# Performance work log

Measured on AMD Instinct MI355X. Metric: run time of the kernel, lower is better.

Reference implementation:

```python
import jax, jax.numpy as jnp
import numpy as np

NUM_CLASSES = 64
FEAT_DIM = 128
LAMBDA_INTER = 1.0
LAMBDA_INTRA = 1.0
MARGIN = 2.0
BATCH = 1_000_000


def setup_inputs() -> dict:
    key = jax.random.key(0)
    k1, k2 = jax.random.split(key)
    features = jax.random.normal(k1, (BATCH, FEAT_DIM), dtype=jnp.float32)
    targets = jax.random.randint(k2, (BATCH,), 0, NUM_CLASSES, dtype=jnp.int32)
    return {"features": features, "targets": targets}


def reference(features, targets):
    C, D = NUM_CLASSES, FEAT_DIM
    B = features.shape[0]
    # per-class scatter-mean centroids
    sums = jax.ops.segment_sum(features, targets, num_segments=C)      # [C, D]
    counts = jax.ops.segment_sum(jnp.ones((B,), features.dtype), targets,
                                 num_segments=C)                        # [C]
    counts = jnp.clip(counts, 1.0)
    centers = sums / counts[:, None]                                    # [C, D]
    # intra-class variance: mean over batch of ||f_i - center_{t_i}||^2
    diff = features - centers[targets]                                   # [B, D]
    intra_loss = jnp.sum(diff * diff) / B
    # inter-class hinge on pairwise squared centroid distances (i < j)
    cd = centers[:, None, :] - centers[None, :, :]                       # [C, C, D]
    d2 = jnp.sum(cd * cd, axis=-1)                                       # [C, C]
    weights = jnp.ones((C, C), features.dtype).at[1, 2].set(2.0)
    upper = jnp.triu(jnp.ones((C, C), features.dtype), k=1)
    hinge = jnp.maximum(MARGIN - d2, 0.0)
    n_pairs = C * (C - 1) // 2
    inter_loss = jnp.sum(weights * hinge * upper) / n_pairs
    return LAMBDA_INTRA * intra_loss + LAMBDA_INTER * inter_loss
```

## Files before the change

kernel.cpp:

```cpp
#include <hip/hip_runtime.h>

#define BATCH 1000000
#define C 64
#define D 128
#define NPAIRS 2016
#define CHUNK 16

__global__ __launch_bounds__(128) void stage1_kernel(
        const float* __restrict__ feat, const int* __restrict__ targets,
        float* __restrict__ pSums, float* __restrict__ pCnt,
        double* __restrict__ pSq, int nB) {
    __shared__ float sAcc[C * D];
    __shared__ double sRed[128];

    const int tid = threadIdx.x;
    for (int i = tid; i < C * D; i += 128) sAcc[i] = 0.0f;
    __syncthreads();

    const int nchunks = BATCH / CHUNK;

    float lsq  = 0.0f;
    float lcnt = 0.0f;

    float fA[CHUNK], fB[CHUNK];
    int   tA[CHUNK], tB[CHUNK];

    int ch = blockIdx.x;
    {
        const int r0 = ch * CHUNK;
#pragma unroll
        for (int u = 0; u < CHUNK; u++) tA[u] = targets[r0 + u];
#pragma unroll
        for (int u = 0; u < CHUNK; u++) fA[u] = feat[(size_t)(r0 + u) * D + tid];
    }

    for (;;) {
        const int chN = ch + nB;
        const bool more = chN < nchunks;
        if (more) {
            const int r0 = chN * CHUNK;
#pragma unroll
            for (int u = 0; u < CHUNK; u++) tB[u] = targets[r0 + u];
#pragma unroll
            for (int u = 0; u < CHUNK; u++) fB[u] = feat[(size_t)(r0 + u) * D + tid];
        }
        __builtin_amdgcn_sched_barrier(0);

#pragma unroll
        for (int u = 0; u < CHUNK; u++) {
            const float f = fA[u];
            lsq  += f * f;
            lcnt += (tA[u] == tid) ? 1.0f : 0.0f;
            sAcc[tA[u] * D + tid] += f;
        }

        if (!more) break;
#pragma unroll
        for (int u = 0; u < CHUNK; u++) { fA[u] = fB[u]; tA[u] = tB[u]; }
        ch = chN;
    }

    __syncthreads();
    sRed[tid] = (double)lsq;
    __syncthreads();
    for (int off = 64; off > 0; off >>= 1) {
        if (tid < off) sRed[tid] += sRed[tid + off];
        __syncthreads();
    }
    if (tid == 0) pSq[blockIdx.x] = sRed[0];

    float* dst = pSums + (size_t)blockIdx.x * (C * D);
    for (int i = tid; i < C * D; i += 128) dst[i] = sAcc[i];
    if (tid < C) pCnt[blockIdx.x * C + tid] = lcnt;
}

__global__ __launch_bounds__(256) void stage2_kernel(
        const float* __restrict__ pSums, const float* __restrict__ pCnt,
        float* __restrict__ centers, float* __restrict__ wc, int nB) {
    __shared__ float scnt[C];
    __shared__ float sred[256];
    const int tid = threadIdx.x;
    const int q = blockIdx.x * 256 + tid;

    {
        const int c = tid & 63;
        const int g = tid >> 6;
        float cp = 0.0f;
        for (int b = g; b < nB; b += 4) cp += pCnt[b * C + c];
        sred[tid] = cp;
        __syncthreads();
        if (tid < C)
            scnt[tid] = sred[tid] + sred[tid + 64] + sred[tid + 128] + sred[tid + 192];
        __syncthreads();
    }

    float s = 0.0f;
#pragma unroll 4
    for (int b = 0; b < nB; b++)
        s += pSums[(size_t)b * (C * D) + q];

    const float cnt = scnt[q >> 7];
    const float cc  = cnt < 1.0f ? 1.0f : cnt;
    const float ctr = s / cc;
    centers[q] = ctr;

    sred[tid] = 2.0f * s * ctr - cnt * ctr * ctr;
    __syncthreads();
    for (int off = 64; off > 0; off >>= 1) {
        if ((tid & 127) < off) sred[tid] += sred[tid + off];
        __syncthreads();
    }
    if ((tid & 127) == 0) wc[q >> 7] = sred[tid];
}

__global__ __launch_bounds__(256) void stage3_kernel(
        const float* __restrict__ centers, const float* __restrict__ wc,
        const double* __restrict__ pSq, float* __restrict__ out, int nB) {
    __shared__ float sCtr[C * 129];
    __shared__ double dred[256];

    const int tid = threadIdx.x;
    for (int idx = tid; idx < C * D; idx += 256) {
        const int i = idx >> 7;
        const int d = idx & 127;
        sCtr[i * 129 + d] = centers[idx];
    }
    __syncthreads();

    float acc = 0.0f;
    for (int q = tid; q < C * C; q += 256) {
        const int i = q >> 6;
        const int j = q & 63;
        if (j > i) {
            const float* ci = sCtr + i * 129;
            const float* cj = sCtr + j * 129;
            float d2 = 0.0f;
            for (int d = 0; d < D; d++) {
                const float df = ci[d] - cj[d];
                d2 += df * df;
            }
            float h = 2.0f - d2;
            if (h < 0.0f) h = 0.0f;
            const float w = (i == 1 && j == 2) ? 2.0f : 1.0f;
            acc += w * h;
        }
    }

    double dacc = 0.0;
    for (int b = tid; b < nB; b += 256) dacc += pSq[b];

    float wacc = 0.0f;
    if (tid < C) wacc = wc[tid];

    dred[tid] = (dacc - (double)wacc) * (1.0 / (double)BATCH)
              + (double)acc * (1.0 / (double)NPAIRS);
    __syncthreads();
    for (int off = 128; off > 0; off >>= 1) {
        if (tid < off) dred[tid] += dred[tid + off];
        __syncthreads();
    }
    if (tid == 0) out[0] = (float)dred[0];
}

extern "C" void kernel_launch(void* const* d_in, const int* in_sizes, int n_in,
                              void* d_out, int out_size, void* d_ws, size_t ws_size,
                              hipStream_t stream) {
    const float* feat    = (const float*)d_in[0];
    const int*   targets = (const int*)d_in[1];
    float* out = (float*)d_out;

    int nB = 1024;
    while (nB > 1) {
        size_t need = (size_t)nB * (C * D + C) * sizeof(float)
                    + (size_t)nB * sizeof(double)
                    + (size_t)(C * D + C) * sizeof(float) + 64;
        if (need <= ws_size) break;
        nB >>= 1;
    }

    float*  pSums   = (float*)d_ws;
    float*  pCnt    = pSums + (size_t)nB * C * D;
    double* pSq     = (double*)(pCnt + (size_t)nB * C);
    float*  centers = (float*)(pSq + nB);
    float*  wcv     = centers + C * D;

    stage1_kernel<<<nB, 128, 0, stream>>>(feat, targets, pSums, pCnt, pSq, nB);
    stage2_kernel<<<(C * D) / 256, 256, 0, stream>>>(pSums, pCnt, centers, wcv, nB);
    stage3_kernel<<<1, 256, 0, stream>>>(centers, wcv, pSq, out, nB);
}
```

Measured before the change: 803.4 us.

## Stream feature chunks into LDS via async global_load_lds double buffering

Replaces the register double-buffered feature loads with asynchronous global-to-LDS transfers (global_load_lds, 16 bytes per lane) into two shared staging buffers. Manual vmcnt waits and barriers overlap the next chunk's transfer with accumulation of the current one. The grid also drops from 1024 to 768 blocks. In exchange it adds LDS pressure and two barriers per chunk, and relies on hand-counted vmcnt values being correct. The target loads still go through registers and now sit on the critical path each iteration.

```diff
diff --git a/kernel.cpp b/kernel.cpp
--- a/kernel.cpp
+++ b/kernel.cpp
@@ -1,63 +1,80 @@
 #include <hip/hip_runtime.h>
+#include <stdint.h>
 
 #define BATCH 1000000
 #define C 64
 #define D 128
 #define NPAIRS 2016
 #define CHUNK 16
+#define NCHUNKS (BATCH / CHUNK)
+
+typedef __attribute__((address_space(1))) const uint8_t ga_u8;
+typedef __attribute__((address_space(3))) uint8_t ls_u8;
+
+__device__ __forceinline__ void stage_chunk(const float* feat, int chunk,
+                                            float* stageBase, int wid, int lane) {
+    const uint8_t* g = (const uint8_t*)feat + (size_t)chunk * (CHUNK * D * 4)
+                     + wid * 4096 + lane * 16;
+    uint8_t* l = (uint8_t*)stageBase + wid * 4096;
+#pragma unroll
+    for (int i = 0; i < 4; i++) {
+        __builtin_amdgcn_global_load_lds((const ga_u8*)(g + i * 1024),
+                                         (ls_u8*)(l + i * 1024), 16, 0, 0);
+    }
+}
 
 __global__ __launch_bounds__(128) void stage1_kernel(
         const float* __restrict__ feat, const int* __restrict__ targets,
         float* __restrict__ pSums, float* __restrict__ pCnt,
         double* __restrict__ pSq, int nB) {
     __shared__ float sAcc[C * D];
+    __shared__ float sStage[2][CHUNK * D];
     __shared__ double sRed[128];
 
-    const int tid = threadIdx.x;
+    const int tid  = threadIdx.x;
+    const int lane = tid & 63;
+    const int wid  = tid >> 6;
+
     for (int i = tid; i < C * D; i += 128) sAcc[i] = 0.0f;
     __syncthreads();
-
-    const int nchunks = BATCH / CHUNK;
 
     float lsq  = 0.0f;
     float lcnt = 0.0f;
 
-    float fA[CHUNK], fB[CHUNK];
-    int   tA[CHUNK], tB[CHUNK];
-
     int ch = blockIdx.x;
-    {
+    stage_chunk(feat, ch, sStage[0], wid, lane);
+
+    int buf = 0;
+    for (;;) {
+        const int chN = ch + nB;
+        const bool more = chN < NCHUNKS;
+
+        int tloc[CHUNK];
         const int r0 = ch * CHUNK;
 #pragma unroll
-        for (int u = 0; u < CHUNK; u++) tA[u] = targets[r0 + u];
-#pragma unroll
-        for (int u = 0; u < CHUNK; u++) fA[u] = feat[(size_t)(r0 + u) * D + tid];
-    }
-
-    for (;;) {
-        const int chN = ch + nB;
-        const bool more = chN < nchunks;
-        if (more) {
-            const int r0 = chN * CHUNK;
-#pragma unroll
-            for (int u = 0; u < CHUNK; u++) tB[u] = targets[r0 + u];
-#pragma unroll
-            for (int u = 0; u < CHUNK; u++) fB[u] = feat[(size_t)(r0 + u) * D + tid];
-        }
-        __builtin_amdgcn_sched_barrier(0);
-
+        for (int u = 0; u < CHUNK; u++) tloc[u] = targets[r0 + u];
+
+        if (more) stage_chunk(feat, chN, sStage[buf ^ 1], wid, lane);
+
+        if (more) asm volatile("s_waitcnt vmcnt(4)" ::: "memory");
+        else      asm volatile("s_waitcnt vmcnt(0)" ::: "memory");
+        __builtin_amdgcn_s_barrier();
+
+        const float* st = sStage[buf];
 #pragma unroll
         for (int u = 0; u < CHUNK; u++) {
-            const float f = fA[u];
+            const int t = tloc[u];
+            const float f = st[u * D + tid];
             lsq  += f * f;
-            lcnt += (tA[u] == tid) ? 1.0f : 0.0f;
-            sAcc[tA[u] * D + tid] += f;
+            lcnt += (t == tid) ? 1.0f : 0.0f;
+            sAcc[t * D + tid] += f;
         }
 
         if (!more) break;
-#pragma unroll
-        for (int u = 0; u < CHUNK; u++) { fA[u] = fB[u]; tA[u] = tB[u]; }
+        asm volatile("s_waitcnt lgkmcnt(0)" ::: "memory");
+        __builtin_amdgcn_s_barrier();
         ch = chN;
+        buf ^= 1;
     }
 
     __syncthreads();
@@ -169,7 +186,7 @@
     const int*   targets = (const int*)d_in[1];
     float* out = (float*)d_out;
 
-    int nB = 1024;
+    int nB = 768;
     while (nB > 1) {
         size_t need = (size_t)nB * (C * D + C) * sizeof(float)
                     + (size_t)nB * sizeof(double)
```

Result: faster. 775.5 us (-3.5%).
